# Kernel tuning notes

Measured on AMD Instinct MI355X. Metric: run time of the kernel, lower is better.

Reference implementation:

```python
import jax, jax.numpy as jnp
import numpy as np

B, N, C, E, M = 16, 4096, 128, 12288, 64  # batch, nodes(seq_len), channels, incidences, hyperedges
NEG_SLOPE = 0.2
MARGIN = 4.2


def setup_inputs() -> dict:
    key = jax.random.key(0)
    k1, k2, k3, k4, k5 = jax.random.split(key, 5)
    x = jax.random.normal(k1, (B, N, C), jnp.float32)
    hyperedge_nodes = jax.random.randint(k2, (E,), 0, N)
    hyperedge_edges = jax.random.randint(k3, (E,), 0, M)
    weight = jax.random.normal(k4, (C, C), jnp.float32) * (1.0 / np.sqrt(C))  # glorot-ish
    att = jax.random.normal(k5, (1, 1, 2 * C), jnp.float32) * 0.1  # heads=1
    return {"x": x, "hyperedge_nodes": hyperedge_nodes, "hyperedge_edges": hyperedge_edges,
            "weight": weight, "att": att}


def _segment_softmax(logits, seg, num_segments):
    # logits: [E, B], softmax within groups of seg (per node)
    smax = jax.ops.segment_max(logits, seg, num_segments=num_segments)
    e = jnp.exp(logits - smax[seg])
    ssum = jax.ops.segment_sum(e, seg, num_segments=num_segments)
    return e / (ssum[seg] + 1e-16)


def reference(x, hyperedge_nodes, hyperedge_edges, weight, att):
    nodes = hyperedge_nodes
    edges = hyperedge_edges
    xw = jnp.matmul(x, weight)            # [B, N, C]
    x1 = jnp.swapaxes(xw, 0, 1)           # [N, B, C]

    x_gath = x1[nodes]                    # [E, B, C] gather by node id
    x_i = x_gath
    # per-hyperedge sum of incident node features (the python dict loop in torch)
    edge_sums = jax.ops.segment_sum(x_gath, edges, num_segments=M)  # [M, B, C]
    x_j = edge_sums[edges]                # [E, B, C]

    # O(M^2) pairwise hyperedge loss (vectorized)
    sq = jnp.sum(edge_sums * edge_sums, axis=-1)          # [M, B]
    norms = jnp.sqrt(sq)                                   # [M, B]
    inner = jnp.einsum('mbc,nbc->mnb', edge_sums, edge_sums)  # [M, M, B]
    cos = inner / (norms[:, None, :] * norms[None, :, :])      # [M, M, B]
    dist = jnp.sqrt(jnp.clip(sq[:, None, :] + sq[None, :, :] - 2.0 * inner, 0.0))
    loss_item = cos * dist + (1.0 - cos) * jnp.maximum(MARGIN - dist, 0.0)  # [M, M, B]
    loss_hyper = jnp.sum(jnp.abs(jnp.mean(loss_item, axis=-1))) / float((M + 1) ** 2)

    # attention per incidence, softmax grouped by node
    alpha = jnp.sum(jnp.concatenate([x_i, x_j], axis=-1) * att, axis=-1)  # [E, B]
    alpha = jax.nn.leaky_relu(alpha, NEG_SLOPE)
    alpha = _segment_softmax(alpha, nodes, N)  # [E, B] (dropout: eval mode, identity)

    ones = jnp.ones((E,), x.dtype)
    D = jax.ops.segment_sum(ones, nodes, num_segments=N)   # node degree
    Bdeg = jax.ops.segment_sum(ones, edges, num_segments=M)
    Bn = jnp.where(Bdeg > 0, 1.0 / Bdeg, 0.0)              # 1/deg, inf -> 0

    # propagate source_to_target: nodes -> hyperedges
    msg1 = Bn[edges][:, None, None] * x1[nodes] * alpha[:, :, None]   # [E, B, C]
    out_e = jax.ops.segment_sum(msg1, edges, num_segments=M)          # [M, B, C]
    # propagate target_to_source: hyperedges -> nodes
    msg2 = D[nodes][:, None, None] * out_e[edges] * alpha[:, :, None]
    out = jax.ops.segment_sum(msg2, nodes, num_segments=N)            # [N, B, C]
    out = jnp.swapaxes(out, 0, 1)                                     # [B, N, C]

    constrain_total = jnp.abs(jnp.mean(x_i - x_j)) + loss_hyper
    return (out, constrain_total)
```

## Files before the change

kernel.cpp:

```cpp
#include <hip/hip_runtime.h>
#include <hip/hip_bf16.h>

#define Bc 16
#define Nn 4096
#define Cc 128
#define Ee 12288
#define Mm 64
#define NEG_SLOPE 0.2f
#define MARGIN 4.2f
#define NCH 32

typedef __attribute__((ext_vector_type(8))) short bfrag;
typedef __attribute__((ext_vector_type(4))) float f32x4;

__device__ inline void split1(float f, unsigned short& h, unsigned short& lo) {
    unsigned u = __float_as_uint(f);
    unsigned hb = u & 0xFFFF0000u;
    float r = f - __uint_as_float(hb);
    unsigned ru = __float_as_uint(r);
    ru += 0x7FFFu + ((ru >> 16) & 1u);
    h = (unsigned short)(u >> 16);
    lo = (unsigned short)(ru >> 16);
}
__device__ inline void split8(const float* f, bfrag& h, bfrag& l) {
#pragma unroll
    for (int j = 0; j < 8; ++j) {
        unsigned short hh, ll;
        split1(f[j], hh, ll);
        h[j] = (short)hh; l[j] = (short)ll;
    }
}

__global__ __launch_bounds__(256) void prep_kernel(const float* __restrict__ w,
                                                   const int* __restrict__ nodes,
                                                   const int* __restrict__ edges,
                                                   unsigned short* __restrict__ wsplit,
                                                   int* __restrict__ deg_n,
                                                   int* __restrict__ deg_m,
                                                   float* __restrict__ Acnt,
                                                   float* __restrict__ AcntT) {
    int blk = blockIdx.x, t = threadIdx.x;
    if (blk < 64) {
        int idx = blk * 256 + t;
        int k = idx >> 7, c = idx & 127;
        float v = w[k * 128 + c];
        unsigned short h, lo;
        split1(v, h, lo);
        int byteoff = c * 256 + ((2 * k) ^ ((c & 7) << 4));
        *(unsigned short*)((char*)wsplit + byteoff) = h;
        *(unsigned short*)((char*)wsplit + 32768 + byteoff) = lo;
    } else {
        int e = (blk - 64) * 256 + t;
        int n = nodes[e], m = edges[e];
        atomicAdd(&deg_n[n], 1);
        atomicAdd(&deg_m[m], 1);
        atomicAdd(&Acnt[m * 4096 + n], 1.0f);
        atomicAdd(&AcntT[n * 64 + m], 1.0f);
    }
}

__global__ __launch_bounds__(256) void gemm_xw(const float* __restrict__ x,
                                               const unsigned short* __restrict__ wsplit,
                                               const float* __restrict__ att,
                                               unsigned short* __restrict__ xwTh,
                                               unsigned short* __restrict__ xwTl,
                                               float* __restrict__ p,
                                               float* __restrict__ S1) {
    __shared__ unsigned short wlds[32768];
    int t = threadIdx.x;
    {
        const float4* g4 = (const float4*)wsplit;
        float4* l4 = (float4*)wlds;
#pragma unroll
        for (int i = 0; i < 16; ++i) l4[i * 256 + t] = g4[i * 256 + t];
    }
    __syncthreads();

    int w = t >> 6, l = t & 63;
    int lrow = l & 15, lk = l >> 4;
    int rowbase = blockIdx.x * 128 + w * 32;

    f32x4 acc[2][8];
#pragma unroll
    for (int ti = 0; ti < 2; ++ti)
#pragma unroll
        for (int tj = 0; tj < 8; ++tj) acc[ti][tj] = (f32x4){0.f, 0.f, 0.f, 0.f};

    for (int ks = 0; ks < 4; ++ks) {
        bfrag bh[8], bl[8];
        int kbyte = (64 * ks + 16 * lk) ^ ((l & 7) << 4);
#pragma unroll
        for (int tj = 0; tj < 8; ++tj) {
            const char* base = (const char*)wlds + (tj * 16 + lrow) * 256 + kbyte;
            bh[tj] = *(const bfrag*)base;
            bl[tj] = *(const bfrag*)(base + 32768);
        }
#pragma unroll
        for (int ti = 0; ti < 2; ++ti) {
            int row = rowbase + ti * 16 + lrow;
            const float4* xp = (const float4*)(x + (size_t)row * 128 + ks * 32 + lk * 8);
            float4 v0 = xp[0], v1 = xp[1];
            float fa[8] = {v0.x, v0.y, v0.z, v0.w, v1.x, v1.y, v1.z, v1.w};
            bfrag ah, al;
#pragma unroll
            for (int j = 0; j < 8; ++j) {
                unsigned short hh, ll;
                split1(fa[j], hh, ll);
                ah[j] = (short)hh; al[j] = (short)ll;
            }
#pragma unroll
            for (int tj = 0; tj < 8; ++tj) {
                acc[ti][tj] = __builtin_amdgcn_mfma_f32_16x16x32_bf16(ah, bh[tj], acc[ti][tj], 0, 0, 0);
                acc[ti][tj] = __builtin_amdgcn_mfma_f32_16x16x32_bf16(ah, bl[tj], acc[ti][tj], 0, 0, 0);
                acc[ti][tj] = __builtin_amdgcn_mfma_f32_16x16x32_bf16(al, bh[tj], acc[ti][tj], 0, 0, 0);
            }
        }
    }

#pragma unroll
    for (int ti = 0; ti < 2; ++ti) {
#pragma unroll
        for (int tj = 0; tj < 8; ++tj) {
            int rr0 = rowbase + ti * 16 + lk * 4;
            int b = rr0 >> 12, n0 = rr0 & 4095;
            int slot = b * 128 + tj * 16 + lrow;
            ushort4 hv, lv;
            split1(acc[ti][tj][0], hv.x, lv.x);
            split1(acc[ti][tj][1], hv.y, lv.y);
            split1(acc[ti][tj][2], hv.z, lv.z);
            split1(acc[ti][tj][3], hv.w, lv.w);
            *(ushort4*)(xwTh + (size_t)slot * 4096 + n0) = hv;
            *(ushort4*)(xwTl + (size_t)slot * 4096 + n0) = lv;
        }
    }
    float aw_[8];
#pragma unroll
    for (int tj = 0; tj < 8; ++tj) aw_[tj] = att[tj * 16 + lrow];
#pragma unroll
    for (int ti = 0; ti < 2; ++ti) {
#pragma unroll
        for (int v = 0; v < 4; ++v) {
            int rr = rowbase + ti * 16 + lk * 4 + v;
            int b = rr >> 12, n = rr & 4095;
            float pd = 0.f, ss = 0.f;
#pragma unroll
            for (int tj = 0; tj < 8; ++tj) {
                float val = acc[ti][tj][v];
                pd += val * aw_[tj];
                ss += val;
            }
#pragma unroll
            for (int m = 1; m < 16; m <<= 1) {
                pd += __shfl_xor(pd, m, 64);
                ss += __shfl_xor(ss, m, 64);
            }
            if (lrow == 0) {
                p[n * 16 + b] = pd;
                atomicAdd(&S1[n], ss);
            }
        }
    }
}

__global__ __launch_bounds__(256) void es_gemm(const float* __restrict__ Acnt,
                                               const unsigned short* __restrict__ xwTh,
                                               const unsigned short* __restrict__ xwTl,
                                               float* __restrict__ es_part) {
    int t = threadIdx.x, w = t >> 6, l = t & 63;
    int lrow = l & 15, lk = l >> 4;
    int slot0 = blockIdx.x * 64;
    int kbase = blockIdx.y * (4096 / NCH);
    f32x4 acc[4];
#pragma unroll
    for (int tj = 0; tj < 4; ++tj) acc[tj] = (f32x4){0.f, 0.f, 0.f, 0.f};
    const float* arow = Acnt + (size_t)(w * 16 + lrow) * 4096;
#pragma unroll
    for (int ks = 0; ks < 4096 / NCH / 32; ++ks) {
        int n0 = kbase + ks * 32 + lk * 8;
        const float* ap = arow + n0;
        bfrag af;
#pragma unroll
        for (int j = 0; j < 8; ++j) af[j] = (short)(__float_as_uint(ap[j]) >> 16);
#pragma unroll
        for (int tj = 0; tj < 4; ++tj) {
            size_t off = (size_t)(slot0 + tj * 16 + lrow) * 4096 + n0;
            bfrag bh = *(const bfrag*)(xwTh + off);
            bfrag bl = *(const bfrag*)(xwTl + off);
            acc[tj] = __builtin_amdgcn_mfma_f32_16x16x32_bf16(af, bh, acc[tj], 0, 0, 0);
            acc[tj] = __builtin_amdgcn_mfma_f32_16x16x32_bf16(af, bl, acc[tj], 0, 0, 0);
        }
    }
    float* dst = es_part + (size_t)blockIdx.y * 64 * 2048;
#pragma unroll
    for (int tj = 0; tj < 4; ++tj) {
        int slot = slot0 + tj * 16 + lrow;
#pragma unroll
        for (int reg = 0; reg < 4; ++reg) {
            int mm = w * 16 + lk * 4 + reg;
            dst[mm * 2048 + slot] = acc[tj][reg];
        }
    }
}

__global__ __launch_bounds__(256) void es_reduce(const float* __restrict__ es_part,
                                                 const float* __restrict__ att,
                                                 float* __restrict__ es,
                                                 float* __restrict__ q,
                                                 float* __restrict__ T) {
    int m = blockIdx.x, t = threadIdx.x;
    float v[8] = {0, 0, 0, 0, 0, 0, 0, 0};
    for (int ch = 0; ch < NCH; ++ch) {
        const float4* src = (const float4*)(es_part + ((size_t)ch * 64 + m) * 2048 + t * 8);
        float4 a = src[0], b4 = src[1];
        v[0] += a.x; v[1] += a.y; v[2] += a.z; v[3] += a.w;
        v[4] += b4.x; v[5] += b4.y; v[6] += b4.z; v[7] += b4.w;
    }
    float4* dst = (float4*)(es + m * 2048 + t * 8);
    dst[0] = make_float4(v[0], v[1], v[2], v[3]);
    dst[1] = make_float4(v[4], v[5], v[6], v[7]);
    int b = t >> 4, c0 = (t & 15) * 8;
    float qd = 0.f, tp = 0.f;
#pragma unroll
    for (int j = 0; j < 8; ++j) {
        qd += v[j] * att[128 + c0 + j];
        tp += v[j];
    }
#pragma unroll
    for (int k = 1; k < 16; k <<= 1) {
        qd += __shfl_xor(qd, k, 64);
        tp += __shfl_xor(tp, k, 64);
    }
    if ((t & 15) == 0) q[m * 16 + b] = qd;
    tp += __shfl_xor(tp, 16, 64);
    tp += __shfl_xor(tp, 32, 64);
    __shared__ float ws4[4];
    if ((t & 63) == 0) ws4[t >> 6] = tp;
    __syncthreads();
    if (t == 0) T[m] = ws4[0] + ws4[1] + ws4[2] + ws4[3];
}

__global__ __launch_bounds__(256) void loss_kernel(const float* __restrict__ es,
                                                   float* __restrict__ loss_part) {
    int m = blockIdx.x, t = threadIdx.x;
    __shared__ float esm[2048];
    __shared__ float sml[16];
    for (int i = t; i < 2048; i += 256) esm[i] = es[m * 2048 + i];
    __syncthreads();
    if (t < 16) {
        float s = 0.f;
        const float* r = esm + t * 128;
        for (int c = 0; c < 128; ++c) s += r[c] * r[c];
        sml[t] = s;
    }
    __syncthreads();
    int n = t >> 2, bq = t & 3;
    float part = 0.f;
#pragma unroll
    for (int u = 0; u < 4; u++) {
        int b = bq * 4 + u;
        float inner = 0.f, sn = 0.f;
        const float* er = es + n * 2048 + b * 128;
        const float* em = esm + b * 128;
        for (int c = 0; c < 128; c += 4) {
            float4 a = *(const float4*)(em + c);
            float4 o = *(const float4*)(er + c);
            inner += a.x * o.x + a.y * o.y + a.z * o.z + a.w * o.w;
            sn += o.x * o.x + o.y * o.y + o.z * o.z + o.w * o.w;
        }
        float sm = sml[b];
        float cosv = inner / (sqrtf(sm) * sqrtf(sn));
        float d2 = sm + sn - 2.f * inner;
        float dist = sqrtf(fmaxf(d2, 0.f));
        part += cosv * dist + (1.f - cosv) * fmaxf(MARGIN - dist, 0.f);
    }
    part += __shfl_xor(part, 1, 64);
    part += __shfl_xor(part, 2, 64);
    float labs = fabsf(part * (1.f / 16.f));
    __shared__ float pl[64];
    if (bq == 0) pl[n] = labs;
    __syncthreads();
    if (t < 64) {
        float v = pl[t];
        for (int k = 1; k < 64; k <<= 1) v += __shfl_xor(v, k, 64);
        if (t == 0) loss_part[m] = v;
    }
}

__global__ __launch_bounds__(256) void alpha_wab(const float* __restrict__ AcntT,
                                                 const float* __restrict__ p,
                                                 const float* __restrict__ q,
                                                 const int* __restrict__ deg_m,
                                                 float* __restrict__ Wa,
                                                 float* __restrict__ Wb) {
    __shared__ float acl[16][68];
    __shared__ float qs[64][16];
    int t = threadIdx.x;
    int n0 = blockIdx.x * 16;
    {
        int row = t >> 4, c4 = (t & 15) * 4;
        *(float4*)&acl[row][c4] = *(const float4*)(AcntT + (size_t)(n0 + row) * 64 + c4);
        int mq = t >> 2, bq4 = (t & 3) * 4;
        *(float4*)&qs[mq][bq4] = *(const float4*)(q + mq * 16 + bq4);
    }
    __syncthreads();
    int b = t & 15, tn = t >> 4;
    int n = n0 + tn;
    float pb = p[n * 16 + b];
    float mx = -1e30f;
    for (int m = 0; m < 64; ++m) {
        if (acl[tn][m] > 0.f) {
            float lg = pb + qs[m][b];
            lg = lg >= 0.f ? lg : NEG_SLOPE * lg;
            mx = fmaxf(mx, lg);
        }
    }
    float ssum = 0.f;
    for (int m = 0; m < 64; ++m) {
        float cnt = acl[tn][m];
        if (cnt > 0.f) {
            float lg = pb + qs[m][b];
            lg = lg >= 0.f ? lg : NEG_SLOPE * lg;
            ssum += cnt * __expf(lg - mx);
        }
    }
    if (ssum == 0.f) return;
    float inv = 1.f / ssum;
    for (int m = 0; m < 64; ++m) {
        float cnt = acl[tn][m];
        if (cnt > 0.f) {
            float lg = pb + qs[m][b];
            lg = lg >= 0.f ? lg : NEG_SLOPE * lg;
            float a = cnt * __expf(lg - mx) * inv;
            Wa[((size_t)b * 64 + m) * 4096 + n] = a;
            Wb[((size_t)b * 4096 + n) * 64 + m] = a / (float)deg_m[m];
        }
    }
}

__global__ __launch_bounds__(256) void oute_gemm(const unsigned short* __restrict__ xwTh,
                                                 const unsigned short* __restrict__ xwTl,
                                                 const float* __restrict__ Wa,
                                                 float* __restrict__ ouT_part) {
    int t = threadIdx.x, w = t >> 6, l = t & 63;
    int lrow = l & 15, lk = l >> 4;
    int slot0 = blockIdx.x * 64;
    int b = slot0 >> 7;
    int kbase = blockIdx.y * (4096 / NCH);
    f32x4 acc[4];
#pragma unroll
    for (int tj = 0; tj < 4; ++tj) acc[tj] = (f32x4){0.f, 0.f, 0.f, 0.f};
    int srow = slot0 + w * 16 + lrow;
    const unsigned short* xh = xwTh + (size_t)srow * 4096;
    const unsigned short* xl = xwTl + (size_t)srow * 4096;
    const float* wab = Wa + (size_t)b * 64 * 4096;
#pragma unroll
    for (int ks = 0; ks < 4096 / NCH / 32; ++ks) {
        int n0 = kbase + ks * 32 + lk * 8;
        bfrag ah = *(const bfrag*)(xh + n0);
        bfrag al = *(const bfrag*)(xl + n0);
#pragma unroll
        for (int tj = 0; tj < 4; ++tj) {
            int mcol = tj * 16 + lrow;
            bfrag wh, wl_;
            split8(wab + (size_t)mcol * 4096 + n0, wh, wl_);
            acc[tj] = __builtin_amdgcn_mfma_f32_16x16x32_bf16(ah, wh, acc[tj], 0, 0, 0);
            acc[tj] = __builtin_amdgcn_mfma_f32_16x16x32_bf16(ah, wl_, acc[tj], 0, 0, 0);
            acc[tj] = __builtin_amdgcn_mfma_f32_16x16x32_bf16(al, wh, acc[tj], 0, 0, 0);
        }
    }
    float* dst = ouT_part + (size_t)blockIdx.y * 2048 * 64;
#pragma unroll
    for (int tj = 0; tj < 4; ++tj) {
        int mcol = tj * 16 + lrow;
#pragma unroll
        for (int reg = 0; reg < 4; ++reg) {
            int slot = slot0 + w * 16 + lk * 4 + reg;
            dst[slot * 64 + mcol] = acc[tj][reg];
        }
    }
}

__global__ __launch_bounds__(256) void oute_reduce(const float* __restrict__ ouT_part,
                                                   float* __restrict__ ouT) {
    int idx = blockIdx.x * 256 + threadIdx.x;
    int slot = idx >> 4, m4 = (idx & 15) * 4;
    float4 s = make_float4(0.f, 0.f, 0.f, 0.f);
    for (int ch = 0; ch < NCH; ++ch) {
        float4 a = *(const float4*)(ouT_part + ((size_t)ch * 2048 + slot) * 64 + m4);
        s.x += a.x; s.y += a.y; s.z += a.z; s.w += a.w;
    }
    *(float4*)(ouT + (size_t)slot * 64 + m4) = s;
}

__global__ __launch_bounds__(256) void out_gemm(const float* __restrict__ Wb,
                                                const float* __restrict__ ouT,
                                                const int* __restrict__ deg_n,
                                                float* __restrict__ out) {
    int t = threadIdx.x, w = t >> 6, l = t & 63;
    int lrow = l & 15, lk = l >> 4;
    int nbase = blockIdx.x * 64 + w * 16;
    int b = blockIdx.y;
    f32x4 acc[8];
#pragma unroll
    for (int tj = 0; tj < 8; ++tj) acc[tj] = (f32x4){0.f, 0.f, 0.f, 0.f};
#pragma unroll
    for (int ks = 0; ks < 2; ++ks) {
        int m0 = ks * 32 + lk * 8;
        bfrag wh, wl;
        int nr = nbase + lrow;
        split8(Wb + ((size_t)b * 4096 + nr) * 64 + m0, wh, wl);
#pragma unroll
        for (int tj = 0; tj < 8; ++tj) {
            int slot = b * 128 + tj * 16 + lrow;
            bfrag oh, ol;
            split8(ouT + (size_t)slot * 64 + m0, oh, ol);
            acc[tj] = __builtin_amdgcn_mfma_f32_16x16x32_bf16(wh, oh, acc[tj], 0, 0, 0);
            acc[tj] = __builtin_amdgcn_mfma_f32_16x16x32_bf16(wh, ol, acc[tj], 0, 0, 0);
            acc[tj] = __builtin_amdgcn_mfma_f32_16x16x32_bf16(wl, oh, acc[tj], 0, 0, 0);
        }
    }
#pragma unroll
    for (int reg = 0; reg < 4; ++reg) {
        int n = nbase + lk * 4 + reg;
        float d = (float)deg_n[n];
#pragma unroll
        for (int tj = 0; tj < 8; ++tj) {
            out[(size_t)b * 524288 + (size_t)n * 128 + tj * 16 + lrow] = d * acc[tj][reg];
        }
    }
}

__global__ __launch_bounds__(256) void finalize_kernel(const int* __restrict__ deg_n,
                                                       const float* __restrict__ S1,
                                                       const int* __restrict__ deg_m,
                                                       const float* __restrict__ T,
                                                       const float* __restrict__ loss_part,
                                                       float* __restrict__ out_scalar) {
    int t = threadIdx.x;
    double a = 0.0;
    for (int n = t; n < 4096; n += 256) a += (double)deg_n[n] * (double)S1[n];
    double bsum = 0.0, lsum = 0.0;
    if (t < 64) {
        bsum = (double)deg_m[t] * (double)T[t];
        lsum = (double)loss_part[t];
    }
    __shared__ double sa[256], sb[256], sl[256];
    sa[t] = a; sb[t] = bsum; sl[t] = lsum;
    __syncthreads();
    for (int s = 128; s > 0; s >>= 1) {
        if (t < s) { sa[t] += sa[t + s]; sb[t] += sb[t + s]; sl[t] += sl[t + s]; }
        __syncthreads();
    }
    if (t == 0) {
        double mean = (sa[0] - sb[0]) / 25165824.0;
        out_scalar[0] = (float)(fabs(mean) + sl[0] / 4225.0);
    }
}

extern "C" void kernel_launch(void* const* d_in, const int* in_sizes, int n_in,
                              void* d_out, int out_size, void* d_ws, size_t ws_size,
                              hipStream_t stream) {
    const float* x = (const float*)d_in[0];
    const int* nodes = (const int*)d_in[1];
    const int* edges = (const int*)d_in[2];
    const float* w = (const float*)d_in[3];
    const float* att = (const float*)d_in[4];
    float* out = (float*)d_out;

    char* ws = (char*)d_ws;
    size_t o = 0;
    unsigned short* xwTh = (unsigned short*)(ws + o); o += (size_t)2048 * 4096 * 2;
    unsigned short* xwTl = (unsigned short*)(ws + o); o += (size_t)2048 * 4096 * 2;
    float* es_part = (float*)(ws + o);  o += (size_t)NCH * Mm * 2048 * 4;
    float* ouT_part = (float*)(ws + o); o += (size_t)NCH * 2048 * Mm * 4;
    size_t zbase = o;
    float* Acnt = (float*)(ws + o);  o += (size_t)Mm * Nn * 4;
    float* AcntT = (float*)(ws + o); o += (size_t)Nn * Mm * 4;
    float* Wa = (float*)(ws + o);    o += (size_t)Bc * Mm * Nn * 4;
    float* Wb = (float*)(ws + o);    o += (size_t)Bc * Nn * Mm * 4;
    int* deg_n = (int*)(ws + o);     o += (size_t)Nn * 4;
    int* deg_m = (int*)(ws + o);     o += (size_t)Mm * 4;
    float* S1 = (float*)(ws + o);    o += (size_t)Nn * 4;
    size_t zlen = o - zbase;
    float* es = (float*)(ws + o);        o += (size_t)Mm * 2048 * 4;
    float* ouT = (float*)(ws + o);       o += (size_t)2048 * Mm * 4;
    float* p = (float*)(ws + o);         o += (size_t)Nn * Bc * 4;
    float* q = (float*)(ws + o);         o += (size_t)Mm * Bc * 4;
    float* T = (float*)(ws + o);         o += (size_t)Mm * 4;
    float* loss_part = (float*)(ws + o); o += (size_t)Mm * 4;
    unsigned short* wsplit = (unsigned short*)(ws + o); o += 65536;

    hipMemsetAsync(ws + zbase, 0, zlen, stream);

    prep_kernel<<<112, 256, 0, stream>>>(w, nodes, edges, wsplit, deg_n, deg_m, Acnt, AcntT);
    gemm_xw<<<512, 256, 0, stream>>>(x, wsplit, att, xwTh, xwTl, p, S1);
    es_gemm<<<dim3(32, NCH), 256, 0, stream>>>(Acnt, xwTh, xwTl, es_part);
    es_reduce<<<Mm, 256, 0, stream>>>(es_part, att, es, q, T);
    loss_kernel<<<Mm, 256, 0, stream>>>(es, loss_part);
    alpha_wab<<<256, 256, 0, stream>>>(AcntT, p, q, deg_m, Wa, Wb);
    oute_gemm<<<dim3(32, NCH), 256, 0, stream>>>(xwTh, xwTl, Wa, ouT_part);
    oute_reduce<<<128, 256, 0, stream>>>(ouT_part, ouT);
    out_gemm<<<dim3(64, 16), 256, 0, stream>>>(Wb, ouT, deg_n, out);
    finalize_kernel<<<1, 256, 0, stream>>>(deg_n, S1, deg_m, T, loss_part, out + (size_t)Bc * Nn * Cc);
}
```

Baseline: 251.9 us.

## Pre-split attention weights into bf16 hi/lo and halve gemm_xw LDS footprint

The attention weight matrices Wa and Wb and the ouT buffer are now written as separate bf16 high and low halves by their producer kernels. The consumer GEMMs load them directly as MFMA fragments instead of reading fp32 and splitting per lane. gemm_xw also stages the split weight in two 64-row halves, halving its LDS use, which may allow more blocks per CU at the cost of an extra barrier and reload. This cuts global traffic and conversion ALU in the consumers, in exchange for scattered 2-byte stores in alpha_wab.

```diff
diff --git a/kernel.cpp b/kernel.cpp
--- a/kernel.cpp
+++ b/kernel.cpp
@@ -21,14 +21,6 @@
     ru += 0x7FFFu + ((ru >> 16) & 1u);
     h = (unsigned short)(u >> 16);
     lo = (unsigned short)(ru >> 16);
-}
-__device__ inline void split8(const float* f, bfrag& h, bfrag& l) {
-#pragma unroll
-    for (int j = 0; j < 8; ++j) {
-        unsigned short hh, ll;
-        split1(f[j], hh, ll);
-        h[j] = (short)hh; l[j] = (short)ll;
-    }
 }
 
 __global__ __launch_bounds__(256) void prep_kernel(const float* __restrict__ w,
@@ -46,9 +38,10 @@
         float v = w[k * 128 + c];
         unsigned short h, lo;
         split1(v, h, lo);
-        int byteoff = c * 256 + ((2 * k) ^ ((c & 7) << 4));
+        int half = k >> 6, kk = k & 63;
+        int byteoff = half * 32768 + c * 128 + ((2 * kk) ^ ((c & 7) << 4));
         *(unsigned short*)((char*)wsplit + byteoff) = h;
-        *(unsigned short*)((char*)wsplit + 32768 + byteoff) = lo;
+        *(unsigned short*)((char*)wsplit + byteoff + 16384) = lo;
     } else {
         int e = (blk - 64) * 256 + t;
         int n = nodes[e], m = edges[e];
@@ -66,16 +59,8 @@
                                                unsigned short* __restrict__ xwTl,
                                                float* __restrict__ p,
                                                float* __restrict__ S1) {
-    __shared__ unsigned short wlds[32768];
+    __shared__ unsigned short wlds[16384];
     int t = threadIdx.x;
-    {
-        const float4* g4 = (const float4*)wsplit;
-        float4* l4 = (float4*)wlds;
-#pragma unroll
-        for (int i = 0; i < 16; ++i) l4[i * 256 + t] = g4[i * 256 + t];
-    }
-    __syncthreads();
-
     int w = t >> 6, l = t & 63;
     int lrow = l & 15, lk = l >> 4;
     int rowbase = blockIdx.x * 128 + w * 32;
@@ -86,35 +71,46 @@
 #pragma unroll
         for (int tj = 0; tj < 8; ++tj) acc[ti][tj] = (f32x4){0.f, 0.f, 0.f, 0.f};
 
-    for (int ks = 0; ks < 4; ++ks) {
-        bfrag bh[8], bl[8];
-        int kbyte = (64 * ks + 16 * lk) ^ ((l & 7) << 4);
-#pragma unroll
-        for (int tj = 0; tj < 8; ++tj) {
-            const char* base = (const char*)wlds + (tj * 16 + lrow) * 256 + kbyte;
-            bh[tj] = *(const bfrag*)base;
-            bl[tj] = *(const bfrag*)(base + 32768);
-        }
-#pragma unroll
-        for (int ti = 0; ti < 2; ++ti) {
-            int row = rowbase + ti * 16 + lrow;
-            const float4* xp = (const float4*)(x + (size_t)row * 128 + ks * 32 + lk * 8);
-            float4 v0 = xp[0], v1 = xp[1];
-            float fa[8] = {v0.x, v0.y, v0.z, v0.w, v1.x, v1.y, v1.z, v1.w};
-            bfrag ah, al;
-#pragma unroll
-            for (int j = 0; j < 8; ++j) {
-                unsigned short hh, ll;
-                split1(fa[j], hh, ll);
-                ah[j] = (short)hh; al[j] = (short)ll;
+    for (int half = 0; half < 2; ++half) {
+        {
+            const float4* g4 = (const float4*)(wsplit + (size_t)half * 16384);
+            float4* l4 = (float4*)wlds;
+#pragma unroll
+            for (int i = 0; i < 8; ++i) l4[i * 256 + t] = g4[i * 256 + t];
+        }
+        __syncthreads();
+#pragma unroll
+        for (int ks2 = 0; ks2 < 2; ++ks2) {
+            bfrag bh[8], bl[8];
+            int kbyte = (64 * ks2 + 16 * lk) ^ ((l & 7) << 4);
+#pragma unroll
+            for (int tj = 0; tj < 8; ++tj) {
+                const char* base = (const char*)wlds + (tj * 16 + lrow) * 128 + kbyte;
+                bh[tj] = *(const bfrag*)base;
+                bl[tj] = *(const bfrag*)(base + 16384);
             }
 #pragma unroll
-            for (int tj = 0; tj < 8; ++tj) {
-                acc[ti][tj] = __builtin_amdgcn_mfma_f32_16x16x32_bf16(ah, bh[tj], acc[ti][tj], 0, 0, 0);
-                acc[ti][tj] = __builtin_amdgcn_mfma_f32_16x16x32_bf16(ah, bl[tj], acc[ti][tj], 0, 0, 0);
-                acc[ti][tj] = __builtin_amdgcn_mfma_f32_16x16x32_bf16(al, bh[tj], acc[ti][tj], 0, 0, 0);
+            for (int ti = 0; ti < 2; ++ti) {
+                int row = rowbase + ti * 16 + lrow;
+                const float4* xp = (const float4*)(x + (size_t)row * 128 + half * 64 + ks2 * 32 + lk * 8);
+                float4 v0 = xp[0], v1 = xp[1];
+                float fa[8] = {v0.x, v0.y, v0.z, v0.w, v1.x, v1.y, v1.z, v1.w};
+                bfrag ah, al;
+#pragma unroll
+                for (int j = 0; j < 8; ++j) {
+                    unsigned short hh, ll;
+                    split1(fa[j], hh, ll);
+                    ah[j] = (short)hh; al[j] = (short)ll;
+                }
+#pragma unroll
+                for (int tj = 0; tj < 8; ++tj) {
+                    acc[ti][tj] = __builtin_amdgcn_mfma_f32_16x16x32_bf16(ah, bh[tj], acc[ti][tj], 0, 0, 0);
+                    acc[ti][tj] = __builtin_amdgcn_mfma_f32_16x16x32_bf16(ah, bl[tj], acc[ti][tj], 0, 0, 0);
+                    acc[ti][tj] = __builtin_amdgcn_mfma_f32_16x16x32_bf16(al, bh[tj], acc[ti][tj], 0, 0, 0);
+                }
             }
         }
+        __syncthreads();
     }
 
 #pragma unroll
@@ -290,8 +286,10 @@
                                                  const float* __restrict__ p,
                                                  const float* __restrict__ q,
                                                  const int* __restrict__ deg_m,
-                                                 float* __restrict__ Wa,
-                                                 float* __restrict__ Wb) {
+                                                 unsigned short* __restrict__ Wah,
+                                                 unsigned short* __restrict__ Wal,
+                                                 unsigned short* __restrict__ Wbh,
+                                                 unsigned short* __restrict__ Wbl) {
     __shared__ float acl[16][68];
     __shared__ float qs[64][16];
     int t = threadIdx.x;
@@ -331,15 +329,22 @@
             float lg = pb + qs[m][b];
             lg = lg >= 0.f ? lg : NEG_SLOPE * lg;
             float a = cnt * __expf(lg - mx) * inv;
-            Wa[((size_t)b * 64 + m) * 4096 + n] = a;
-            Wb[((size_t)b * 4096 + n) * 64 + m] = a / (float)deg_m[m];
+            unsigned short h, lo;
+            split1(a, h, lo);
+            size_t ia = ((size_t)b * 64 + m) * 4096 + n;
+            Wah[ia] = h; Wal[ia] = lo;
+            float wbv = a / (float)deg_m[m];
+            split1(wbv, h, lo);
+            size_t ib = ((size_t)b * 4096 + n) * 64 + m;
+            Wbh[ib] = h; Wbl[ib] = lo;
         }
     }
 }
 
 __global__ __launch_bounds__(256) void oute_gemm(const unsigned short* __restrict__ xwTh,
                                                  const unsigned short* __restrict__ xwTl,
-                                                 const float* __restrict__ Wa,
+                                                 const unsigned short* __restrict__ Wah,
+                                                 const unsigned short* __restrict__ Wal,
                                                  float* __restrict__ ouT_part) {
     int t = threadIdx.x, w = t >> 6, l = t & 63;
     int lrow = l & 15, lk = l >> 4;
@@ -352,7 +357,8 @@
     int srow = slot0 + w * 16 + lrow;
     const unsigned short* xh = xwTh + (size_t)srow * 4096;
     const unsigned short* xl = xwTl + (size_t)srow * 4096;
-    const float* wab = Wa + (size_t)b * 64 * 4096;
+    const unsigned short* wah = Wah + (size_t)b * 64 * 4096;
+    const unsigned short* wal = Wal + (size_t)b * 64 * 4096;
 #pragma unroll
     for (int ks = 0; ks < 4096 / NCH / 32; ++ks) {
         int n0 = kbase + ks * 32 + lk * 8;
@@ -361,8 +367,8 @@
 #pragma unroll
         for (int tj = 0; tj < 4; ++tj) {
             int mcol = tj * 16 + lrow;
-            bfrag wh, wl_;
-            split8(wab + (size_t)mcol * 4096 + n0, wh, wl_);
+            bfrag wh = *(const bfrag*)(wah + (size_t)mcol * 4096 + n0);
+            bfrag wl_ = *(const bfrag*)(wal + (size_t)mcol * 4096 + n0);
             acc[tj] = __builtin_amdgcn_mfma_f32_16x16x32_bf16(ah, wh, acc[tj], 0, 0, 0);
             acc[tj] = __builtin_amdgcn_mfma_f32_16x16x32_bf16(ah, wl_, acc[tj], 0, 0, 0);
             acc[tj] = __builtin_amdgcn_mfma_f32_16x16x32_bf16(al, wh, acc[tj], 0, 0, 0);
@@ -381,7 +387,8 @@
 }
 
 __global__ __launch_bounds__(256) void oute_reduce(const float* __restrict__ ouT_part,
-                                                   float* __restrict__ ouT) {
+                                                   unsigned short* __restrict__ ouTh,
+                                                   unsigned short* __restrict__ ouTl) {
     int idx = blockIdx.x * 256 + threadIdx.x;
     int slot = idx >> 4, m4 = (idx & 15) * 4;
     float4 s = make_float4(0.f, 0.f, 0.f, 0.f);
@@ -389,11 +396,19 @@
         float4 a = *(const float4*)(ouT_part + ((size_t)ch * 2048 + slot) * 64 + m4);
         s.x += a.x; s.y += a.y; s.z += a.z; s.w += a.w;
     }
-    *(float4*)(ouT + (size_t)slot * 64 + m4) = s;
-}
-
-__global__ __launch_bounds__(256) void out_gemm(const float* __restrict__ Wb,
-                                                const float* __restrict__ ouT,
+    ushort4 hv, lv;
+    split1(s.x, hv.x, lv.x);
+    split1(s.y, hv.y, lv.y);
+    split1(s.z, hv.z, lv.z);
+    split1(s.w, hv.w, lv.w);
+    *(ushort4*)(ouTh + (size_t)slot * 64 + m4) = hv;
+    *(ushort4*)(ouTl + (size_t)slot * 64 + m4) = lv;
+}
+
+__global__ __launch_bounds__(256) void out_gemm(const unsigned short* __restrict__ Wbh,
+                                                const unsigned short* __restrict__ Wbl,
+                                                const unsigned short* __restrict__ ouTh,
+                                                const unsigned short* __restrict__ ouTl,
                                                 const int* __restrict__ deg_n,
                                                 float* __restrict__ out) {
     int t = threadIdx.x, w = t >> 6, l = t & 63;
@@ -406,14 +421,14 @@
 #pragma unroll
     for (int ks = 0; ks < 2; ++ks) {
         int m0 = ks * 32 + lk * 8;
-        bfrag wh, wl;
         int nr = nbase + lrow;
-        split8(Wb + ((size_t)b * 4096 + nr) * 64 + m0, wh, wl);
+        bfrag wh = *(const bfrag*)(Wbh + ((size_t)b * 4096 + nr) * 64 + m0);
+        bfrag wl = *(const bfrag*)(Wbl + ((size_t)b * 4096 + nr) * 64 + m0);
 #pragma unroll
         for (int tj = 0; tj < 8; ++tj) {
             int slot = b * 128 + tj * 16 + lrow;
-            bfrag oh, ol;
-            split8(ouT + (size_t)slot * 64 + m0, oh, ol);
+            bfrag oh = *(const bfrag*)(ouTh + (size_t)slot * 64 + m0);
+            bfrag ol = *(const bfrag*)(ouTl + (size_t)slot * 64 + m0);
             acc[tj] = __builtin_amdgcn_mfma_f32_16x16x32_bf16(wh, oh, acc[tj], 0, 0, 0);
             acc[tj] = __builtin_amdgcn_mfma_f32_16x16x32_bf16(wh, ol, acc[tj], 0, 0, 0);
             acc[tj] = __builtin_amdgcn_mfma_f32_16x16x32_bf16(wl, oh, acc[tj], 0, 0, 0);
@@ -476,14 +491,17 @@
     size_t zbase = o;
     float* Acnt = (float*)(ws + o);  o += (size_t)Mm * Nn * 4;
     float* AcntT = (float*)(ws + o); o += (size_t)Nn * Mm * 4;
-    float* Wa = (float*)(ws + o);    o += (size_t)Bc * Mm * Nn * 4;
-    float* Wb = (float*)(ws + o);    o += (size_t)Bc * Nn * Mm * 4;
+    unsigned short* Wah = (unsigned short*)(ws + o); o += (size_t)Bc * Mm * Nn * 2;
+    unsigned short* Wal = (unsigned short*)(ws + o); o += (size_t)Bc * Mm * Nn * 2;
+    unsigned short* Wbh = (unsigned short*)(ws + o); o += (size_t)Bc * Nn * Mm * 2;
+    unsigned short* Wbl = (unsigned short*)(ws + o); o += (size_t)Bc * Nn * Mm * 2;
     int* deg_n = (int*)(ws + o);     o += (size_t)Nn * 4;
     int* deg_m = (int*)(ws + o);     o += (size_t)Mm * 4;
     float* S1 = (float*)(ws + o);    o += (size_t)Nn * 4;
     size_t zlen = o - zbase;
     float* es = (float*)(ws + o);        o += (size_t)Mm * 2048 * 4;
-    float* ouT = (float*)(ws + o);       o += (size_t)2048 * Mm * 4;
+    unsigned short* ouTh = (unsigned short*)(ws + o); o += (size_t)2048 * Mm * 2;
+    unsigned short* ouTl = (unsigned short*)(ws + o); o += (size_t)2048 * Mm * 2;
     float* p = (float*)(ws + o);         o += (size_t)Nn * Bc * 4;
     float* q = (float*)(ws + o);         o += (size_t)Mm * Bc * 4;
     float* T = (float*)(ws + o);         o += (size_t)Mm * 4;
@@ -497,9 +515,9 @@
     es_gemm<<<dim3(32, NCH), 256, 0, stream>>>(Acnt, xwTh, xwTl, es_part);
     es_reduce<<<Mm, 256, 0, stream>>>(es_part, att, es, q, T);
     loss_kernel<<<Mm, 256, 0, stream>>>(es, loss_part);
-    alpha_wab<<<256, 256, 0, stream>>>(AcntT, p, q, deg_m, Wa, Wb);
-    oute_gemm<<<dim3(32, NCH), 256, 0, stream>>>(xwTh, xwTl, Wa, ouT_part);
-    oute_reduce<<<128, 256, 0, stream>>>(ouT_part, ouT);
-    out_gemm<<<dim3(64, 16), 256, 0, stream>>>(Wb, ouT, deg_n, out);
+    alpha_wab<<<256, 256, 0, stream>>>(AcntT, p, q, deg_m, Wah, Wal, Wbh, Wbl);
+    oute_gemm<<<dim3(32, NCH), 256, 0, stream>>>(xwTh, xwTl, Wah, Wal, ouT_part);
+    oute_reduce<<<128, 256, 0, stream>>>(ouT_part, ouTh, ouTl);
+    out_gemm<<<dim3(64, 16), 256, 0, stream>>>(Wbh, Wbl, ouTh, ouTl, deg_n, out);
     finalize_kernel<<<1, 256, 0, stream>>>(deg_n, S1, deg_m, T, loss_part, out + (size_t)Bc * Nn * Cc);
 }
```

After: 250.8 us. Within noise of the previous version (-0.4%).
